# Performance work log

Measured on AMD Instinct MI355X. Metric: run time of the kernel, lower is better.

Reference implementation:

```python
import jax, jax.numpy as jnp
import numpy as np

N = 50000
E = 800000
IN_DIM = 256
HID = 256
OUT_DIM = 2


def setup_inputs() -> dict:
    key = jax.random.key(0)
    ks = jax.random.split(key, 10)
    x = jax.random.normal(ks[0], (N, IN_DIM), dtype=jnp.float32)
    edge_index = jax.random.randint(ks[1], (2, E), 0, N, dtype=jnp.int64)
    # Glorot-ish scaling so activations stay well-conditioned through 4 layers
    def w(k, fan_in, fan_out):
        return jax.random.normal(k, (fan_in, fan_out), dtype=jnp.float32) / jnp.sqrt(jnp.float32(fan_in))
    return {
        "x": x,
        "edge_index": edge_index,
        "W0": w(ks[2], IN_DIM, HID), "b0": jnp.zeros((HID,), jnp.float32),
        "W1": w(ks[3], HID, HID),    "b1": jnp.zeros((HID,), jnp.float32),
        "W2": w(ks[4], HID, HID),    "b2": jnp.zeros((HID,), jnp.float32),
        "W3": w(ks[5], HID, OUT_DIM), "b3": jnp.zeros((OUT_DIM,), jnp.float32),
    }


def _gcn_norm(edge_index, n, dtype):
    # PyG gcn_norm with self-loops: deg over destination, norm = d^-1/2[src]*d^-1/2[dst]
    loops = jnp.arange(n, dtype=edge_index.dtype)
    src = jnp.concatenate([edge_index[0], loops])
    dst = jnp.concatenate([edge_index[1], loops])
    deg = jax.ops.segment_sum(jnp.ones_like(dst, dtype=dtype), dst, num_segments=n)
    dis = deg ** -0.5  # deg >= 1 due to self-loops
    norm = dis[src] * dis[dst]
    return src, dst, norm


def reference(x, edge_index, W0, b0, W1, b1, W2, b2, W3, b3):
    n = x.shape[0]
    src, dst, norm = _gcn_norm(edge_index, n, x.dtype)

    def conv(h, W, b):
        h = h @ W                              # [N, F_out] dense GEMM
        msg = h[src] * norm[:, None]           # edge-gather + scale
        agg = jax.ops.segment_sum(msg, dst, num_segments=n)  # scatter-add
        return agg + b

    h = jax.nn.relu(conv(x, W0, b0))
    h = jax.nn.relu(conv(h, W1, b1))
    h = jax.nn.relu(conv(h, W2, b2))
    return conv(h, W3, b3)
```

## Files before the change

kernel.cpp:

```cpp
#include <hip/hip_runtime.h>

#define N_NODES 50000
#define N_EDGES 800000

static inline int cdiv(int a, int b) { return (a + b - 1) / b; }

typedef __attribute__((ext_vector_type(8))) short bf16x8;
typedef __attribute__((ext_vector_type(4))) float f32x4;

static __device__ __forceinline__ unsigned short f2bf(float f) {
    unsigned int u = __float_as_uint(f);
    unsigned int r = (u + 0x7FFF + ((u >> 16) & 1)) >> 16;
    return (unsigned short)r;
}
static __device__ __forceinline__ float bf2f(unsigned short h) {
    return __uint_as_float((unsigned int)h << 16);
}
static __device__ __forceinline__ float bf_lo(unsigned int u) { return __uint_as_float(u << 16); }
static __device__ __forceinline__ float bf_hi(unsigned int u) { return __uint_as_float(u & 0xFFFF0000u); }


static __device__ __forceinline__ void acc8(float* acc, uint4 v, float wgt) {
    acc[0] += wgt * bf_lo(v.x);
    acc[1] += wgt * bf_hi(v.x);
    acc[2] += wgt * bf_lo(v.y);
    acc[3] += wgt * bf_hi(v.y);
    acc[4] += wgt * bf_lo(v.z);
    acc[5] += wgt * bf_hi(v.z);
    acc[6] += wgt * bf_lo(v.w);
    acc[7] += wgt * bf_hi(v.w);
}


__global__ void k_init_cnt(int* cnt, int n) {
    int i = blockIdx.x * 256 + threadIdx.x;
    if (i < n) cnt[i] = 1;
}

__global__ void k_count(const int* __restrict__ edst, int* cnt, int e) {
    int i = blockIdx.x * 256 + threadIdx.x;
    if (i < e) atomicAdd(&cnt[edst[i]], 1);
}

__global__ __launch_bounds__(256) void k_scan1(const int* __restrict__ cnt,
                                               int* __restrict__ row_ptr,
                                               float* __restrict__ dis,
                                               int* __restrict__ blk, int n) {
    __shared__ int sums[256];
    int t = threadIdx.x;
    int base = blockIdx.x * 1024 + t * 4;
    int c0 = 0, c1 = 0, c2 = 0, c3 = 0;
    if (base + 3 < n) {
        int4 v = *(const int4*)(cnt + base);
        c0 = v.x; c1 = v.y; c2 = v.z; c3 = v.w;
    } else {
        if (base + 0 < n) c0 = cnt[base + 0];
        if (base + 1 < n) c1 = cnt[base + 1];
        if (base + 2 < n) c2 = cnt[base + 2];
        if (base + 3 < n) c3 = cnt[base + 3];
    }
    int s = c0 + c1 + c2 + c3;
    sums[t] = s;
    __syncthreads();
    int x = s;
    for (int off = 1; off < 256; off <<= 1) {
        int y = (t >= off) ? sums[t - off] : 0;
        __syncthreads();
        x += y;
        sums[t] = x;
        __syncthreads();
    }
    int excl = x - s;
    if (base + 0 < n) { row_ptr[base + 0] = excl;                dis[base + 0] = rsqrtf((float)c0); }
    if (base + 1 < n) { row_ptr[base + 1] = excl + c0;           dis[base + 1] = rsqrtf((float)c1); }
    if (base + 2 < n) { row_ptr[base + 2] = excl + c0 + c1;      dis[base + 2] = rsqrtf((float)c2); }
    if (base + 3 < n) { row_ptr[base + 3] = excl + c0 + c1 + c2; dis[base + 3] = rsqrtf((float)c3); }
    if (t == 255) blk[blockIdx.x] = x;
}

__global__ __launch_bounds__(256) void k_scan2(int* __restrict__ blk,
                                               int* __restrict__ row_ptr_n, int nb) {
    __shared__ int sums[256];
    int t = threadIdx.x;
    int s = (t < nb) ? blk[t] : 0;
    sums[t] = s;
    __syncthreads();
    int x = s;
    for (int off = 1; off < 256; off <<= 1) {
        int y = (t >= off) ? sums[t - off] : 0;
        __syncthreads();
        x += y;
        sums[t] = x;
        __syncthreads();
    }
    if (t < nb) blk[t] = x - s;
    if (t == 255) row_ptr_n[0] = x;
}

__global__ __launch_bounds__(256) void k_scan3(int* __restrict__ row_ptr,
                                               int* __restrict__ pos,
                                               const int* __restrict__ blk, int n) {
    int base = blockIdx.x * 1024 + threadIdx.x * 4;
    int off = blk[blockIdx.x];
#pragma unroll
    for (int i = 0; i < 4; ++i) {
        int idx = base + i;
        if (idx < n) {
            int v = row_ptr[idx] + off;
            row_ptr[idx] = v;
            pos[idx] = v;
        }
    }
}

__global__ void k_fill(const int* __restrict__ esrc, const int* __restrict__ edst,
                       int* pos, const float* __restrict__ dis,
                       int* src_s, float* norm_s, int e, int n) {
    int i = blockIdx.x * 256 + threadIdx.x;
    if (i < e) {
        int s = esrc[i], d = edst[i];
        int p = atomicAdd(&pos[d], 1);
        src_s[p] = s;
        norm_s[p] = dis[s] * dis[d];
    } else if (i < e + n) {
        int v = i - e;
        int p = atomicAdd(&pos[v], 1);
        src_s[p] = v;
        float d = dis[v];
        norm_s[p] = d * d;
    }
}


__global__ __launch_bounds__(256) void k_split_w3(const float* __restrict__ W0,
                                                  const float* __restrict__ W1,
                                                  const float* __restrict__ W2,
                                                  unsigned short* __restrict__ Wth,
                                                  unsigned short* __restrict__ Wtl) {
    int layer = blockIdx.x >> 8;
    int n = blockIdx.x & 255;
    int p = threadIdx.x;
    const float* W = layer == 0 ? W0 : (layer == 1 ? W1 : W2);
    int k = p;
    if (layer != 0) {
        int pl = p & 63;
        k = (p & ~63) + (pl & 3) * 16 + (pl >> 2);
    }
    float v = W[(size_t)k * 256 + n];
    unsigned short h = f2bf(v);
    size_t o = (size_t)layer * 65536 + (size_t)n * 256 + p;
    Wth[o] = h;
    Wtl[o] = f2bf(v - bf2f(h));
}


__global__ __launch_bounds__(256) void k_split_a(const float* __restrict__ X,
                                                 unsigned short* __restrict__ Xh,
                                                 unsigned short* __restrict__ Xl, long total4) {
    long i = (long)blockIdx.x * 256 + threadIdx.x;
    if (i >= total4) return;
    float4 v = *(const float4*)(X + i * 4);
    ushort4 h, l;
    h.x = f2bf(v.x); l.x = f2bf(v.x - bf2f(h.x));
    h.y = f2bf(v.y); l.y = f2bf(v.y - bf2f(h.y));
    h.z = f2bf(v.z); l.z = f2bf(v.z - bf2f(h.z));
    h.w = f2bf(v.w); l.w = f2bf(v.w - bf2f(h.w));
    *(ushort4*)(Xh + i * 4) = h;
    *(ushort4*)(Xl + i * 4) = l;
}


#define GEMM_RB 196

__global__ __launch_bounds__(256) void k_gemm_mfma(const unsigned short* __restrict__ Ah,
                                                   const unsigned short* __restrict__ Al,
                                                   const unsigned short* __restrict__ Wth,
                                                   const unsigned short* __restrict__ Wtl,
                                                   unsigned short* __restrict__ C, int M) {
    __shared__ unsigned short Wh[64][264];
    __shared__ unsigned short Wl[64][264];
    int rowblk = blockIdx.x % GEMM_RB;
    int colblk = blockIdx.x / GEMM_RB;
    int c0 = colblk * 64;
    int m0 = rowblk * 256;
    int t = threadIdx.x;

    {
        int r = t >> 2;
        int k0 = (t & 3) * 64;
        const unsigned short* gh = Wth + (size_t)(c0 + r) * 256 + k0;
        const unsigned short* gl = Wtl + (size_t)(c0 + r) * 256 + k0;
        unsigned short* lh = &Wh[r][k0];
        unsigned short* ll = &Wl[r][k0];
#pragma unroll
        for (int i = 0; i < 8; ++i) {
            *(uint4*)(lh + i * 8) = *(const uint4*)(gh + i * 8);
            *(uint4*)(ll + i * 8) = *(const uint4*)(gl + i * 8);
        }
    }
    __syncthreads();

    int lane = t & 63, wave = t >> 6;
    int quad = lane >> 4, l16 = lane & 15;

    const unsigned short* aph[4];
    const unsigned short* apl[4];
#pragma unroll
    for (int mt = 0; mt < 4; ++mt) {
        int m = m0 + wave * 64 + mt * 16 + l16;
        if (m >= M) m = M - 1;
        aph[mt] = Ah + (size_t)m * 256;
        apl[mt] = Al + (size_t)m * 256;
    }

    f32x4 acc[4][4];
#pragma unroll
    for (int i = 0; i < 4; ++i)
#pragma unroll
        for (int j = 0; j < 4; ++j) acc[i][j] = (f32x4){0.f, 0.f, 0.f, 0.f};

#pragma unroll 2
    for (int kc = 0; kc < 8; ++kc) {
        int ko = kc * 32 + quad * 8;
        bf16x8 ahf[4], alf[4];
#pragma unroll
        for (int mt = 0; mt < 4; ++mt) {
            ahf[mt] = *(const bf16x8*)(aph[mt] + ko);
            alf[mt] = *(const bf16x8*)(apl[mt] + ko);
        }
#pragma unroll
        for (int nt = 0; nt < 4; ++nt) {
            bf16x8 bh = *(const bf16x8*)&Wh[nt * 16 + l16][ko];
            bf16x8 bl = *(const bf16x8*)&Wl[nt * 16 + l16][ko];
#pragma unroll
            for (int mt = 0; mt < 4; ++mt) {
                acc[mt][nt] = __builtin_amdgcn_mfma_f32_16x16x32_bf16(ahf[mt], bh, acc[mt][nt], 0, 0, 0);
                acc[mt][nt] = __builtin_amdgcn_mfma_f32_16x16x32_bf16(ahf[mt], bl, acc[mt][nt], 0, 0, 0);
                acc[mt][nt] = __builtin_amdgcn_mfma_f32_16x16x32_bf16(alf[mt], bh, acc[mt][nt], 0, 0, 0);
            }
        }
    }

#pragma unroll
    for (int mt = 0; mt < 4; ++mt) {
#pragma unroll
        for (int r = 0; r < 4; ++r) {
            int row = m0 + wave * 64 + mt * 16 + quad * 4 + r;
            if (row < M) {
                ushort4 sv;
                sv.x = f2bf(acc[mt][0][r]);
                sv.y = f2bf(acc[mt][1][r]);
                sv.z = f2bf(acc[mt][2][r]);
                sv.w = f2bf(acc[mt][3][r]);
                *(ushort4*)(C + (size_t)row * 256 + c0 + l16 * 4) = sv;
            }
        }
    }
}


__global__ __launch_bounds__(256) void k_agg256(const unsigned short* __restrict__ t,
                                                const int* __restrict__ row_ptr,
                                                const int* __restrict__ src_s,
                                                const float* __restrict__ norm_s,
                                                const float* __restrict__ bias,
                                                unsigned short* __restrict__ outh,
                                                unsigned short* __restrict__ outl, int n) {
    int lane = threadIdx.x & 63;
    int wave = threadIdx.x >> 6;
    int node = blockIdx.x * 4 + wave;
    if (node >= n) return;
    int half = lane >> 5;
    int fl = lane & 31;
    int beg = row_ptr[node], end = row_ptr[node + 1];
    float acc[8] = {};
    const unsigned short* tp = t + fl * 8;

    int e = beg + half;
    for (; e + 6 < end; e += 8) {
        int s0 = src_s[e], s1 = src_s[e + 2], s2 = src_s[e + 4], s3 = src_s[e + 6];
        float w0 = norm_s[e], w1 = norm_s[e + 2], w2 = norm_s[e + 4], w3 = norm_s[e + 6];
        uint4 v0 = *(const uint4*)(tp + (size_t)s0 * 256);
        uint4 v1 = *(const uint4*)(tp + (size_t)s1 * 256);
        uint4 v2 = *(const uint4*)(tp + (size_t)s2 * 256);
        uint4 v3 = *(const uint4*)(tp + (size_t)s3 * 256);
        acc8(acc, v0, w0); acc8(acc, v1, w1); acc8(acc, v2, w2); acc8(acc, v3, w3);
    }
    for (; e + 2 < end; e += 4) {
        int s0 = src_s[e], s1 = src_s[e + 2];
        float w0 = norm_s[e], w1 = norm_s[e + 2];
        uint4 v0 = *(const uint4*)(tp + (size_t)s0 * 256);
        uint4 v1 = *(const uint4*)(tp + (size_t)s1 * 256);
        acc8(acc, v0, w0); acc8(acc, v1, w1);
    }
    if (e < end) {
        int s0 = src_s[e];
        float w0 = norm_s[e];
        uint4 v0 = *(const uint4*)(tp + (size_t)s0 * 256);
        acc8(acc, v0, w0);
    }

#pragma unroll
    for (int i = 0; i < 8; ++i) acc[i] += __shfl_xor(acc[i], 32);

    if (half == 0) {
        ushort4 h0, h1, l0, l1;
#pragma unroll
        for (int j = 0; j < 8; ++j) {
            int cb = (fl >> 3) * 64 + (j & 3) * 16 + (fl & 7) * 2 + (j >> 2);
            float v = acc[j] + bias[cb];
            v = v > 0.f ? v : 0.f;
            unsigned short h = f2bf(v);
            unsigned short l = f2bf(v - bf2f(h));
            if (j == 0) { h0.x = h; l0.x = l; }
            else if (j == 1) { h0.y = h; l0.y = l; }
            else if (j == 2) { h0.z = h; l0.z = l; }
            else if (j == 3) { h0.w = h; l0.w = l; }
            else if (j == 4) { h1.x = h; l1.x = l; }
            else if (j == 5) { h1.y = h; l1.y = l; }
            else if (j == 6) { h1.z = h; l1.z = l; }
            else { h1.w = h; l1.w = l; }
        }
        unsigned short* oh = outh + (size_t)node * 256 + fl * 8;
        unsigned short* ol = outl + (size_t)node * 256 + fl * 8;
        *(ushort4*)(oh + 0) = h0;
        *(ushort4*)(oh + 4) = h1;
        *(ushort4*)(ol + 0) = l0;
        *(ushort4*)(ol + 4) = l1;
    }
}


__global__ __launch_bounds__(256) void k_gemm_out2(const unsigned short* __restrict__ Hh,
                                                   const unsigned short* __restrict__ Hl,
                                                   const float* __restrict__ W3,
                                                   float* __restrict__ t2, int n) {
    int lane = threadIdx.x & 63;
    int wave = threadIdx.x >> 6;
    int row = blockIdx.x * 4 + wave;
    if (row >= n) return;
    ushort4 ah = *(const ushort4*)(Hh + (size_t)row * 256 + lane * 4);
    ushort4 al = *(const ushort4*)(Hl + (size_t)row * 256 + lane * 4);
    float v[4];
    v[0] = bf2f(ah.x) + bf2f(al.x);
    v[1] = bf2f(ah.y) + bf2f(al.y);
    v[2] = bf2f(ah.z) + bf2f(al.z);
    v[3] = bf2f(ah.w) + bf2f(al.w);
    float s0 = 0.f, s1 = 0.f;
#pragma unroll
    for (int i = 0; i < 4; ++i) {
        int c = (lane >> 4) * 64 + i * 16 + (lane & 15);
        float2 w = *(const float2*)(W3 + (size_t)c * 2);
        s0 += v[i] * w.x;
        s1 += v[i] * w.y;
    }
#pragma unroll
    for (int off = 32; off > 0; off >>= 1) {
        s0 += __shfl_down(s0, off);
        s1 += __shfl_down(s1, off);
    }
    if (lane == 0) {
        t2[(size_t)row * 2 + 0] = s0;
        t2[(size_t)row * 2 + 1] = s1;
    }
}

__global__ void k_agg2(const float* __restrict__ t2,
                       const int* __restrict__ row_ptr,
                       const int* __restrict__ src_s,
                       const float* __restrict__ norm_s,
                       const float* __restrict__ b3,
                       float* __restrict__ out, int n) {
    int node = blockIdx.x * 256 + threadIdx.x;
    if (node >= n) return;
    int beg = row_ptr[node], end = row_ptr[node + 1];
    float a0 = 0.f, a1 = 0.f;
    for (int e = beg; e < end; ++e) {
        int s = src_s[e];
        float w = norm_s[e];
        float2 v = *(const float2*)(t2 + (size_t)s * 2);
        a0 += w * v.x;
        a1 += w * v.y;
    }
    out[(size_t)node * 2 + 0] = a0 + b3[0];
    out[(size_t)node * 2 + 1] = a1 + b3[1];
}


extern "C" void kernel_launch(void* const* d_in, const int* in_sizes, int n_in,
                              void* d_out, int out_size, void* d_ws, size_t ws_size,
                              hipStream_t stream) {
    const int N = N_NODES, E = N_EDGES;
    const float* x  = (const float*)d_in[0];
    const int* ei   = (const int*)d_in[1];
    const int* esrc = ei;
    const int* edst = ei + E;
    const float* W0 = (const float*)d_in[2];
    const float* b0 = (const float*)d_in[3];
    const float* W1 = (const float*)d_in[4];
    const float* b1 = (const float*)d_in[5];
    const float* W2 = (const float*)d_in[6];
    const float* b2 = (const float*)d_in[7];
    const float* W3 = (const float*)d_in[8];
    const float* b3 = (const float*)d_in[9];
    float* out = (float*)d_out;

    unsigned short* Ahh = (unsigned short*)d_ws;
    unsigned short* All = Ahh + (size_t)N * 256;
    unsigned short* Tb  = All + (size_t)N * 256;
    unsigned short* Wth = Tb + (size_t)N * 256;
    unsigned short* Wtl = Wth + 3 * 65536;
    float* t2     = (float*)(Wtl + 3 * 65536);
    float* dis    = t2 + (size_t)N * 2;
    float* norm_s = dis + N;
    int*   cnt    = (int*)(norm_s + (E + N));
    int*   row_ptr= cnt + N;
    int*   pos    = row_ptr + (N + 1);
    int*   src_s  = pos + N;
    int*   blk    = src_s + (E + N);

    const int NB = cdiv(N, 1024);

    k_init_cnt<<<cdiv(N, 256), 256, 0, stream>>>(cnt, N);
    k_count<<<cdiv(E, 256), 256, 0, stream>>>(edst, cnt, E);
    k_scan1<<<NB, 256, 0, stream>>>(cnt, row_ptr, dis, blk, N);
    k_scan2<<<1, 256, 0, stream>>>(blk, row_ptr + N, NB);
    k_scan3<<<NB, 256, 0, stream>>>(row_ptr, pos, blk, N);
    k_fill<<<cdiv(E + N, 256), 256, 0, stream>>>(esrc, edst, pos, dis, src_s, norm_s, E, N);

    const int ggrid = GEMM_RB * 4;
    const int agrid = cdiv(N, 4);
    const long total4 = (long)N * 64;

    k_split_a<<<cdiv((int)total4, 256), 256, 0, stream>>>(x, Ahh, All, total4);
    k_split_w3<<<768, 256, 0, stream>>>(W0, W1, W2, Wth, Wtl);

    k_gemm_mfma<<<ggrid, 256, 0, stream>>>(Ahh, All, Wth, Wtl, Tb, N);
    k_agg256<<<agrid, 256, 0, stream>>>(Tb, row_ptr, src_s, norm_s, b0, Ahh, All, N);
    k_gemm_mfma<<<ggrid, 256, 0, stream>>>(Ahh, All, Wth + 65536, Wtl + 65536, Tb, N);
    k_agg256<<<agrid, 256, 0, stream>>>(Tb, row_ptr, src_s, norm_s, b1, Ahh, All, N);
    k_gemm_mfma<<<ggrid, 256, 0, stream>>>(Ahh, All, Wth + 2 * 65536, Wtl + 2 * 65536, Tb, N);
    k_agg256<<<agrid, 256, 0, stream>>>(Tb, row_ptr, src_s, norm_s, b2, Ahh, All, N);
    k_gemm_out2<<<agrid, 256, 0, stream>>>(Ahh, All, W3, t2, N);
    k_agg2<<<cdiv(N, 256), 256, 0, stream>>>(t2, row_ptr, src_s, norm_s, b3, out, N);
}
```

Measured before the change: 545.3 us.

## Store GEMM output in 32-column slices and aggregate per slice

The GEMM now writes its bf16 output in a sliced layout: eight column slices of 32 features, each stored contiguously across all nodes. The aggregation kernel is split into eight slice passes, with one wave per node per slice and 4 edges handled in parallel by 16 lanes each. The goal is to keep each slice's gathered working set (about 3.2 MB) cache-resident so the random neighbor gathers hit L2/MALL. The cost is eight times more blocks, narrow 4-byte gathers per lane, and re-reading row_ptr, src_s and norm_s once per slice.

After: 856.1 us. 57.0% more time.

```diff
diff --git a/kernel.cpp b/kernel.cpp
--- a/kernel.cpp
+++ b/kernel.cpp
@@ -19,16 +19,9 @@
 static __device__ __forceinline__ float bf_lo(unsigned int u) { return __uint_as_float(u << 16); }
 static __device__ __forceinline__ float bf_hi(unsigned int u) { return __uint_as_float(u & 0xFFFF0000u); }
 
-
-static __device__ __forceinline__ void acc8(float* acc, uint4 v, float wgt) {
-    acc[0] += wgt * bf_lo(v.x);
-    acc[1] += wgt * bf_hi(v.x);
-    acc[2] += wgt * bf_lo(v.y);
-    acc[3] += wgt * bf_hi(v.y);
-    acc[4] += wgt * bf_lo(v.z);
-    acc[5] += wgt * bf_hi(v.z);
-    acc[6] += wgt * bf_lo(v.w);
-    acc[7] += wgt * bf_hi(v.w);
+static __device__ __forceinline__ int logc(int p) {
+    int pl = p & 63;
+    return (p & ~63) + (pl & 3) * 16 + (pl >> 2);
 }
 
 
@@ -141,11 +134,7 @@
     int n = blockIdx.x & 255;
     int p = threadIdx.x;
     const float* W = layer == 0 ? W0 : (layer == 1 ? W1 : W2);
-    int k = p;
-    if (layer != 0) {
-        int pl = p & 63;
-        k = (p & ~63) + (pl & 3) * 16 + (pl >> 2);
-    }
+    int k = (layer != 0) ? logc(p) : p;
     float v = W[(size_t)k * 256 + n];
     unsigned short h = f2bf(v);
     size_t o = (size_t)layer * 65536 + (size_t)n * 256 + p;
@@ -241,6 +230,8 @@
         }
     }
 
+    int pcol = c0 + l16 * 4;
+    unsigned short* cbase = C + (size_t)(pcol >> 5) * ((size_t)M * 32) + (pcol & 31);
 #pragma unroll
     for (int mt = 0; mt < 4; ++mt) {
 #pragma unroll
@@ -252,81 +243,64 @@
                 sv.y = f2bf(acc[mt][1][r]);
                 sv.z = f2bf(acc[mt][2][r]);
                 sv.w = f2bf(acc[mt][3][r]);
-                *(ushort4*)(C + (size_t)row * 256 + c0 + l16 * 4) = sv;
+                *(ushort4*)(cbase + (size_t)row * 32) = sv;
             }
         }
     }
 }
 
 
-__global__ __launch_bounds__(256) void k_agg256(const unsigned short* __restrict__ t,
-                                                const int* __restrict__ row_ptr,
-                                                const int* __restrict__ src_s,
-                                                const float* __restrict__ norm_s,
-                                                const float* __restrict__ bias,
-                                                unsigned short* __restrict__ outh,
-                                                unsigned short* __restrict__ outl, int n) {
+__global__ __launch_bounds__(256) void k_agg_sliced(const unsigned short* __restrict__ t,
+                                                    const int* __restrict__ row_ptr,
+                                                    const int* __restrict__ src_s,
+                                                    const float* __restrict__ norm_s,
+                                                    const float* __restrict__ bias,
+                                                    unsigned short* __restrict__ outh,
+                                                    unsigned short* __restrict__ outl,
+                                                    int n, int bps) {
+    int slice = blockIdx.x / bps;
+    int nblk = blockIdx.x % bps;
     int lane = threadIdx.x & 63;
-    int wave = threadIdx.x >> 6;
-    int node = blockIdx.x * 4 + wave;
+    int wv = threadIdx.x >> 6;
+    int node = nblk * 4 + wv;
     if (node >= n) return;
-    int half = lane >> 5;
-    int fl = lane & 31;
+    int eo = lane >> 4;
+    int ql = lane & 15;
+
+    const unsigned short* tp = t + (size_t)slice * ((size_t)n * 32) + ql * 2;
     int beg = row_ptr[node], end = row_ptr[node + 1];
-    float acc[8] = {};
-    const unsigned short* tp = t + fl * 8;
-
-    int e = beg + half;
-    for (; e + 6 < end; e += 8) {
-        int s0 = src_s[e], s1 = src_s[e + 2], s2 = src_s[e + 4], s3 = src_s[e + 6];
-        float w0 = norm_s[e], w1 = norm_s[e + 2], w2 = norm_s[e + 4], w3 = norm_s[e + 6];
-        uint4 v0 = *(const uint4*)(tp + (size_t)s0 * 256);
-        uint4 v1 = *(const uint4*)(tp + (size_t)s1 * 256);
-        uint4 v2 = *(const uint4*)(tp + (size_t)s2 * 256);
-        uint4 v3 = *(const uint4*)(tp + (size_t)s3 * 256);
-        acc8(acc, v0, w0); acc8(acc, v1, w1); acc8(acc, v2, w2); acc8(acc, v3, w3);
-    }
-    for (; e + 2 < end; e += 4) {
-        int s0 = src_s[e], s1 = src_s[e + 2];
-        float w0 = norm_s[e], w1 = norm_s[e + 2];
-        uint4 v0 = *(const uint4*)(tp + (size_t)s0 * 256);
-        uint4 v1 = *(const uint4*)(tp + (size_t)s1 * 256);
-        acc8(acc, v0, w0); acc8(acc, v1, w1);
-    }
-    if (e < end) {
-        int s0 = src_s[e];
-        float w0 = norm_s[e];
-        uint4 v0 = *(const uint4*)(tp + (size_t)s0 * 256);
-        acc8(acc, v0, w0);
-    }
-
-#pragma unroll
-    for (int i = 0; i < 8; ++i) acc[i] += __shfl_xor(acc[i], 32);
-
-    if (half == 0) {
-        ushort4 h0, h1, l0, l1;
-#pragma unroll
-        for (int j = 0; j < 8; ++j) {
-            int cb = (fl >> 3) * 64 + (j & 3) * 16 + (fl & 7) * 2 + (j >> 2);
-            float v = acc[j] + bias[cb];
-            v = v > 0.f ? v : 0.f;
-            unsigned short h = f2bf(v);
-            unsigned short l = f2bf(v - bf2f(h));
-            if (j == 0) { h0.x = h; l0.x = l; }
-            else if (j == 1) { h0.y = h; l0.y = l; }
-            else if (j == 2) { h0.z = h; l0.z = l; }
-            else if (j == 3) { h0.w = h; l0.w = l; }
-            else if (j == 4) { h1.x = h; l1.x = l; }
-            else if (j == 5) { h1.y = h; l1.y = l; }
-            else if (j == 6) { h1.z = h; l1.z = l; }
-            else { h1.w = h; l1.w = l; }
-        }
-        unsigned short* oh = outh + (size_t)node * 256 + fl * 8;
-        unsigned short* ol = outl + (size_t)node * 256 + fl * 8;
-        *(ushort4*)(oh + 0) = h0;
-        *(ushort4*)(oh + 4) = h1;
-        *(ushort4*)(ol + 0) = l0;
-        *(ushort4*)(ol + 4) = l1;
+    float a0 = 0.f, a1 = 0.f;
+
+    int e = beg;
+#pragma unroll 2
+    for (; e + 3 < end; e += 4) {
+        int s = src_s[e + eo];
+        float w = norm_s[e + eo];
+        unsigned int v = *(const unsigned int*)(tp + (size_t)s * 32);
+        a0 += w * bf_lo(v);
+        a1 += w * bf_hi(v);
+    }
+    if (e + eo < end) {
+        int s = src_s[e + eo];
+        float w = norm_s[e + eo];
+        unsigned int v = *(const unsigned int*)(tp + (size_t)s * 32);
+        a0 += w * bf_lo(v);
+        a1 += w * bf_hi(v);
+    }
+
+    a0 += __shfl_xor(a0, 16); a0 += __shfl_xor(a0, 32);
+    a1 += __shfl_xor(a1, 16); a1 += __shfl_xor(a1, 32);
+
+    if (eo == 0) {
+        int p = slice * 32 + ql * 2;
+        float v0 = a0 + bias[logc(p)];
+        float v1 = a1 + bias[logc(p + 1)];
+        v0 = v0 > 0.f ? v0 : 0.f;
+        v1 = v1 > 0.f ? v1 : 0.f;
+        unsigned short h0 = f2bf(v0), l0 = f2bf(v0 - bf2f(h0));
+        unsigned short h1 = f2bf(v1), l1 = f2bf(v1 - bf2f(h1));
+        *(unsigned int*)(outh + (size_t)node * 256 + p) = (unsigned int)h0 | ((unsigned int)h1 << 16);
+        *(unsigned int*)(outl + (size_t)node * 256 + p) = (unsigned int)l0 | ((unsigned int)l1 << 16);
     }
 }
 
@@ -349,7 +323,7 @@
     float s0 = 0.f, s1 = 0.f;
 #pragma unroll
     for (int i = 0; i < 4; ++i) {
-        int c = (lane >> 4) * 64 + i * 16 + (lane & 15);
+        int c = logc(lane * 4 + i);
         float2 w = *(const float2*)(W3 + (size_t)c * 2);
         s0 += v[i] * w.x;
         s1 += v[i] * w.y;
@@ -429,18 +403,19 @@
     k_fill<<<cdiv(E + N, 256), 256, 0, stream>>>(esrc, edst, pos, dis, src_s, norm_s, E, N);
 
     const int ggrid = GEMM_RB * 4;
-    const int agrid = cdiv(N, 4);
+    const int bps = cdiv(N, 4);
+    const int agrid = 8 * bps;
     const long total4 = (long)N * 64;
 
     k_split_a<<<cdiv((int)total4, 256), 256, 0, stream>>>(x, Ahh, All, total4);
     k_split_w3<<<768, 256, 0, stream>>>(W0, W1, W2, Wth, Wtl);
 
     k_gemm_mfma<<<ggrid, 256, 0, stream>>>(Ahh, All, Wth, Wtl, Tb, N);
-    k_agg256<<<agrid, 256, 0, stream>>>(Tb, row_ptr, src_s, norm_s, b0, Ahh, All, N);
+    k_agg_sliced<<<agrid, 256, 0, stream>>>(Tb, row_ptr, src_s, norm_s, b0, Ahh, All, N, bps);
     k_gemm_mfma<<<ggrid, 256, 0, stream>>>(Ahh, All, Wth + 65536, Wtl + 65536, Tb, N);
-    k_agg256<<<agrid, 256, 0, stream>>>(Tb, row_ptr, src_s, norm_s, b1, Ahh, All, N);
+    k_agg_sliced<<<agrid, 256, 0, stream>>>(Tb, row_ptr, src_s, norm_s, b1, Ahh, All, N, bps);
     k_gemm_mfma<<<ggrid, 256, 0, stream>>>(Ahh, All, Wth + 2 * 65536, Wtl + 2 * 65536, Tb, N);
-    k_agg256<<<agrid, 256, 0, stream>>>(Tb, row_ptr, src_s, norm_s, b2, Ahh, All, N);
-    k_gemm_out2<<<agrid, 256, 0, stream>>>(Ahh, All, W3, t2, N);
+    k_agg_sliced<<<agrid, 256, 0, stream>>>(Tb, row_ptr, src_s, norm_s, b2, Ahh, All, N, bps);
+    k_gemm_out2<<<agrid / 8, 256, 0, stream>>>(Ahh, All, W3, t2, N);
     k_agg2<<<cdiv(N, 256), 256, 0, stream>>>(t2, row_ptr, src_s, norm_s, b3, out, N);
 }
```

## Restructure GEMM so each block computes all output columns for 128 rows

Applied to the files above, without the earlier changes.

The GEMM grid changes from a 2D split (row blocks × 4 column blocks) to one block per 128 rows that loops over all four 64-column tiles, reloading each W tile into shared memory. Each block's A rows are now read from global memory once per column tile by the same block, which may keep them in L1/L2 instead of being fetched by four separate blocks. The trade-offs are extra syncthreads and W reloads per block, smaller per-wave tiles (2x4 instead of 4x4), and a serial column loop. Column permutation indexing is also refactored into a shared logc helper.

Measured after the change: 552.3 us. About the same (+1.3%).

```diff
diff --git a/kernel.cpp b/kernel.cpp
--- a/kernel.cpp
+++ b/kernel.cpp
@@ -19,6 +19,10 @@
 static __device__ __forceinline__ float bf_lo(unsigned int u) { return __uint_as_float(u << 16); }
 static __device__ __forceinline__ float bf_hi(unsigned int u) { return __uint_as_float(u & 0xFFFF0000u); }
 
+static __device__ __forceinline__ int logc(int p) {
+    int pl = p & 63;
+    return (p & ~63) + (pl & 3) * 16 + (pl >> 2);
+}
 
 static __device__ __forceinline__ void acc8(float* acc, uint4 v, float wgt) {
     acc[0] += wgt * bf_lo(v.x);
@@ -141,11 +145,7 @@
     int n = blockIdx.x & 255;
     int p = threadIdx.x;
     const float* W = layer == 0 ? W0 : (layer == 1 ? W1 : W2);
-    int k = p;
-    if (layer != 0) {
-        int pl = p & 63;
-        k = (p & ~63) + (pl & 3) * 16 + (pl >> 2);
-    }
+    int k = (layer != 0) ? logc(p) : p;
     float v = W[(size_t)k * 256 + n];
     unsigned short h = f2bf(v);
     size_t o = (size_t)layer * 65536 + (size_t)n * 256 + p;
@@ -170,8 +170,6 @@
 }
 
 
-#define GEMM_RB 196
-
 __global__ __launch_bounds__(256) void k_gemm_mfma(const unsigned short* __restrict__ Ah,
                                                    const unsigned short* __restrict__ Al,
                                                    const unsigned short* __restrict__ Wth,
@@ -179,80 +177,82 @@
                                                    unsigned short* __restrict__ C, int M) {
     __shared__ unsigned short Wh[64][264];
     __shared__ unsigned short Wl[64][264];
-    int rowblk = blockIdx.x % GEMM_RB;
-    int colblk = blockIdx.x / GEMM_RB;
-    int c0 = colblk * 64;
-    int m0 = rowblk * 256;
+    int m0 = blockIdx.x * 128;
     int t = threadIdx.x;
-
-    {
-        int r = t >> 2;
-        int k0 = (t & 3) * 64;
-        const unsigned short* gh = Wth + (size_t)(c0 + r) * 256 + k0;
-        const unsigned short* gl = Wtl + (size_t)(c0 + r) * 256 + k0;
-        unsigned short* lh = &Wh[r][k0];
-        unsigned short* ll = &Wl[r][k0];
-#pragma unroll
-        for (int i = 0; i < 8; ++i) {
-            *(uint4*)(lh + i * 8) = *(const uint4*)(gh + i * 8);
-            *(uint4*)(ll + i * 8) = *(const uint4*)(gl + i * 8);
-        }
-    }
-    __syncthreads();
-
     int lane = t & 63, wave = t >> 6;
     int quad = lane >> 4, l16 = lane & 15;
 
-    const unsigned short* aph[4];
-    const unsigned short* apl[4];
-#pragma unroll
-    for (int mt = 0; mt < 4; ++mt) {
-        int m = m0 + wave * 64 + mt * 16 + l16;
+    const unsigned short* aph[2];
+    const unsigned short* apl[2];
+#pragma unroll
+    for (int mt = 0; mt < 2; ++mt) {
+        int m = m0 + wave * 32 + mt * 16 + l16;
         if (m >= M) m = M - 1;
         aph[mt] = Ah + (size_t)m * 256;
         apl[mt] = Al + (size_t)m * 256;
     }
 
-    f32x4 acc[4][4];
-#pragma unroll
-    for (int i = 0; i < 4; ++i)
-#pragma unroll
-        for (int j = 0; j < 4; ++j) acc[i][j] = (f32x4){0.f, 0.f, 0.f, 0.f};
-
-#pragma unroll 2
-    for (int kc = 0; kc < 8; ++kc) {
-        int ko = kc * 32 + quad * 8;
-        bf16x8 ahf[4], alf[4];
-#pragma unroll
-        for (int mt = 0; mt < 4; ++mt) {
-            ahf[mt] = *(const bf16x8*)(aph[mt] + ko);
-            alf[mt] = *(const bf16x8*)(apl[mt] + ko);
-        }
-#pragma unroll
-        for (int nt = 0; nt < 4; ++nt) {
-            bf16x8 bh = *(const bf16x8*)&Wh[nt * 16 + l16][ko];
-            bf16x8 bl = *(const bf16x8*)&Wl[nt * 16 + l16][ko];
-#pragma unroll
-            for (int mt = 0; mt < 4; ++mt) {
-                acc[mt][nt] = __builtin_amdgcn_mfma_f32_16x16x32_bf16(ahf[mt], bh, acc[mt][nt], 0, 0, 0);
-                acc[mt][nt] = __builtin_amdgcn_mfma_f32_16x16x32_bf16(ahf[mt], bl, acc[mt][nt], 0, 0, 0);
-                acc[mt][nt] = __builtin_amdgcn_mfma_f32_16x16x32_bf16(alf[mt], bh, acc[mt][nt], 0, 0, 0);
+    int sr = t >> 2;
+    int sk0 = (t & 3) * 64;
+
+#pragma unroll 1
+    for (int ct = 0; ct < 4; ++ct) {
+        int c0 = ct * 64;
+        __syncthreads();
+        {
+            const unsigned short* gh = Wth + (size_t)(c0 + sr) * 256 + sk0;
+            const unsigned short* gl = Wtl + (size_t)(c0 + sr) * 256 + sk0;
+            unsigned short* lh = &Wh[sr][sk0];
+            unsigned short* ll = &Wl[sr][sk0];
+#pragma unroll
+            for (int i = 0; i < 8; ++i) {
+                *(uint4*)(lh + i * 8) = *(const uint4*)(gh + i * 8);
+                *(uint4*)(ll + i * 8) = *(const uint4*)(gl + i * 8);
             }
         }
-    }
-
-#pragma unroll
-    for (int mt = 0; mt < 4; ++mt) {
-#pragma unroll
-        for (int r = 0; r < 4; ++r) {
-            int row = m0 + wave * 64 + mt * 16 + quad * 4 + r;
-            if (row < M) {
-                ushort4 sv;
-                sv.x = f2bf(acc[mt][0][r]);
-                sv.y = f2bf(acc[mt][1][r]);
-                sv.z = f2bf(acc[mt][2][r]);
-                sv.w = f2bf(acc[mt][3][r]);
-                *(ushort4*)(C + (size_t)row * 256 + c0 + l16 * 4) = sv;
+        __syncthreads();
+
+        f32x4 acc[2][4];
+#pragma unroll
+        for (int i = 0; i < 2; ++i)
+#pragma unroll
+            for (int j = 0; j < 4; ++j) acc[i][j] = (f32x4){0.f, 0.f, 0.f, 0.f};
+
+#pragma unroll 2
+        for (int kc = 0; kc < 8; ++kc) {
+            int ko = kc * 32 + quad * 8;
+            bf16x8 ahf[2], alf[2];
+#pragma unroll
+            for (int mt = 0; mt < 2; ++mt) {
+                ahf[mt] = *(const bf16x8*)(aph[mt] + ko);
+                alf[mt] = *(const bf16x8*)(apl[mt] + ko);
+            }
+#pragma unroll
+            for (int nt = 0; nt < 4; ++nt) {
+                bf16x8 bh = *(const bf16x8*)&Wh[nt * 16 + l16][ko];
+                bf16x8 bl = *(const bf16x8*)&Wl[nt * 16 + l16][ko];
+#pragma unroll
+                for (int mt = 0; mt < 2; ++mt) {
+                    acc[mt][nt] = __builtin_amdgcn_mfma_f32_16x16x32_bf16(ahf[mt], bh, acc[mt][nt], 0, 0, 0);
+                    acc[mt][nt] = __builtin_amdgcn_mfma_f32_16x16x32_bf16(ahf[mt], bl, acc[mt][nt], 0, 0, 0);
+                    acc[mt][nt] = __builtin_amdgcn_mfma_f32_16x16x32_bf16(alf[mt], bh, acc[mt][nt], 0, 0, 0);
+                }
+            }
+        }
+
+#pragma unroll
+        for (int mt = 0; mt < 2; ++mt) {
+#pragma unroll
+            for (int r = 0; r < 4; ++r) {
+                int row = m0 + wave * 32 + mt * 16 + quad * 4 + r;
+                if (row < M) {
+                    ushort4 sv;
+                    sv.x = f2bf(acc[mt][0][r]);
+                    sv.y = f2bf(acc[mt][1][r]);
+                    sv.z = f2bf(acc[mt][2][r]);
+                    sv.w = f2bf(acc[mt][3][r]);
+                    *(ushort4*)(C + (size_t)row * 256 + c0 + l16 * 4) = sv;
+                }
             }
         }
     }
@@ -307,7 +307,7 @@
         ushort4 h0, h1, l0, l1;
 #pragma unroll
         for (int j = 0; j < 8; ++j) {
-            int cb = (fl >> 3) * 64 + (j & 3) * 16 + (fl & 7) * 2 + (j >> 2);
+            int cb = logc(fl * 8 + j);
             float v = acc[j] + bias[cb];
             v = v > 0.f ? v : 0.f;
             unsigned short h = f2bf(v);
@@ -349,7 +349,7 @@
     float s0 = 0.f, s1 = 0.f;
 #pragma unroll
     for (int i = 0; i < 4; ++i) {
-        int c = (lane >> 4) * 64 + i * 16 + (lane & 15);
+        int c = logc(lane * 4 + i);
         float2 w = *(const float2*)(W3 + (size_t)c * 2);
         s0 += v[i] * w.x;
         s1 += v[i] * w.y;
@@ -428,7 +428,7 @@
     k_scan3<<<NB, 256, 0, stream>>>(row_ptr, pos, blk, N);
     k_fill<<<cdiv(E + N, 256), 256, 0, stream>>>(esrc, edst, pos, dis, src_s, norm_s, E, N);
 
-    const int ggrid = GEMM_RB * 4;
+    const int ggrid = cdiv(N, 128);
     const int agrid = cdiv(N, 4);
     const long total4 = (long)N * 64;
 
```
